# Kernel optimization log

Measured on AMD Instinct MI355X. Metric: run time of the kernel, lower is better.

The kernel has to match this reference:

```python
import jax, jax.numpy as jnp
import numpy as np

EPS = 1e-08


def setup_inputs() -> dict:
    key = jax.random.key(0)
    k1, k2, k3 = jax.random.split(key, 3)
    B_img, B_txt, D = 8192, 8192, 512
    img_feature = jax.random.normal(k1, (B_img, D), dtype=jnp.float32)
    text_feature = jax.random.normal(k2, (B_txt, D), dtype=jnp.float32)
    text_lens = jax.random.randint(k3, (B_txt,), 1, 40, dtype=jnp.int32)
    return {"img_feature": img_feature, "text_feature": text_feature, "text_lens": text_lens}


def reference(img_feature, text_feature, text_lens):
    # Pairwise cosine similarity: equivalent to the original expand+mul+sum,
    # expressed as a GEMM of the raw features followed by norm division.
    # w12[i,j] = <img_i, txt_j>; sim = w12 / max(|img_i|*|txt_j|, eps)
    w12 = jnp.einsum('id,jd->ij', img_feature, text_feature)  # [B_img, B_txt]
    w1 = jnp.linalg.norm(img_feature, axis=-1)                # [B_img]
    w2 = jnp.linalg.norm(text_feature, axis=-1)               # [B_txt]
    denom = jnp.maximum(w1[:, None] * w2[None, :], EPS)
    return w12 / denom
```

## Files before the change

kernel.cpp:

```cpp
#include <hip/hip_runtime.h>
#include <hip/hip_bf16.h>

#define M 8192
#define N 8192
#define K 512
#define BM 256
#define BN 128
#define BK 32
#define NT (K / BK)
#define EPSV 1e-8f

typedef __attribute__((ext_vector_type(8))) short bf16x8;
typedef __attribute__((ext_vector_type(4))) float f32x4;
typedef __attribute__((ext_vector_type(8))) unsigned short us8;

__device__ inline void gload_lds16(const void* g, void* l) {
  __builtin_amdgcn_global_load_lds(
      (const __attribute__((address_space(1))) unsigned int*)g,
      (__attribute__((address_space(3))) unsigned int*)l, 16, 0, 0);
}

#define BARRIER()                          \
  do {                                     \
    asm volatile("" ::: "memory");         \
    __builtin_amdgcn_s_barrier();          \
    asm volatile("" ::: "memory");         \
  } while (0)

__global__ __launch_bounds__(256) void prep_kernel(const float* __restrict__ img,
                                                   const float* __restrict__ txt,
                                                   unsigned short* __restrict__ Abf,
                                                   unsigned short* __restrict__ Bbf,
                                                   float* __restrict__ w1,
                                                   float* __restrict__ w2) {
  const int half = blockIdx.x >> 11;
  const int lb = blockIdx.x & 2047;
  const float* in = half ? txt : img;
  unsigned short* outb = half ? Bbf : Abf;
  float* norms = half ? w2 : w1;

  const int gw = (lb * 256 + threadIdx.x) >> 6;
  const int lane = threadIdx.x & 63;
  const float4* rp4 = (const float4*)(in + (size_t)gw * K);
  float4 v0 = rp4[lane * 2];
  float4 v1 = rp4[lane * 2 + 1];
  float ss = v0.x * v0.x + v0.y * v0.y + v0.z * v0.z + v0.w * v0.w +
             v1.x * v1.x + v1.y * v1.y + v1.z * v1.z + v1.w * v1.w;
  float f[8] = {v0.x, v0.y, v0.z, v0.w, v1.x, v1.y, v1.z, v1.w};
  us8 o;
#pragma unroll
  for (int i = 0; i < 8; ++i) {
    __hip_bfloat16 b = __float2bfloat16(f[i]);
    o[i] = *(unsigned short*)&b;
  }
  *(us8*)(outb + (size_t)gw * K + lane * 8) = o;
#pragma unroll
  for (int off = 32; off > 0; off >>= 1) ss += __shfl_down(ss, off, 64);
  if (lane == 0) norms[gw] = sqrtf(ss);
}

__global__ __launch_bounds__(512, 4) void gemm_kernel(const unsigned short* __restrict__ A,
                                                      const unsigned short* __restrict__ B,
                                                      const float* __restrict__ w1,
                                                      const float* __restrict__ w2,
                                                      float* __restrict__ C) {
  __shared__ __align__(128) unsigned short As[2][BM * BK];
  __shared__ __align__(128) unsigned short Bs[3][BN * BK];

  const int tid = threadIdx.x;
  const int wave = tid >> 6;
  const int lane = tid & 63;
  const int wr = wave >> 1;
  const int wc = wave & 1;
  const int fr = lane & 15;
  const int fq = lane >> 4;

  const int xcd = blockIdx.x & 7;
  const int idx = blockIdx.x >> 3;
  const int bRow = (idx >> 3) * BM;
  const int bCol = (xcd * 8 + (idx & 7)) * BN;

  const int srow = lane >> 2;
  const int scol = (lane & 3) * 8;

  auto stageA = [&](int buf, int kt) {
#pragma unroll
    for (int c = 0; c < 2; ++c)
      gload_lds16(A + (size_t)(bRow + c * 128 + wave * 16 + srow) * K + kt * BK + scol,
                  (char*)&As[buf][0] + (c * 128 + wave * 16) * 64);
  };
  auto stageB = [&](int buf, int kt) {
    gload_lds16(B + (size_t)(bCol + wave * 16 + srow) * K + kt * BK + scol,
                (char*)&Bs[buf][0] + wave * 16 * 64);
  };
  auto ldA = [&](int buf, int r) -> bf16x8 {
    return *(const bf16x8*)((const char*)&As[buf][0] + r * 64 + fq * 16);
  };
  auto ldB = [&](int buf, int r) -> bf16x8 {
    return *(const bf16x8*)((const char*)&Bs[buf][0] + r * 64 + fq * 16);
  };

  f32x4 acc[4][4] = {};
  bf16x8 a[4], b[4];

  stageA(0, 0);
  stageB(0, 0);
  stageB(1, 1);
  asm volatile("s_waitcnt vmcnt(1)" ::: "memory");
  BARRIER();

#pragma unroll
  for (int t = 0; t < NT; ++t) {
    const int cur = t & 1, nxt = cur ^ 1;
    const int bc = t % 3, b2 = (t + 2) % 3;

#pragma unroll
    for (int m = 0; m < 4; ++m) a[m] = ldA(cur, wr * 64 + m * 16 + fr);
    b[0] = ldB(bc, wc * 64 + fr);
    b[1] = ldB(bc, wc * 64 + 16 + fr);
    if (t + 1 < NT) stageA(nxt, t + 1);
    BARRIER();
    __builtin_amdgcn_s_setprio(1);
#pragma unroll
    for (int m = 0; m < 4; ++m)
#pragma unroll
      for (int n = 0; n < 2; ++n)
        acc[m][n] = __builtin_amdgcn_mfma_f32_16x16x32_bf16(a[m], b[n], acc[m][n], 0, 0, 0);
    __builtin_amdgcn_s_setprio(0);
    BARRIER();

    b[2] = ldB(bc, wc * 64 + 32 + fr);
    b[3] = ldB(bc, wc * 64 + 48 + fr);
    if (t + 2 < NT) stageB(b2, t + 2);
    BARRIER();
    __builtin_amdgcn_s_setprio(1);
#pragma unroll
    for (int m = 0; m < 4; ++m)
#pragma unroll
      for (int n = 2; n < 4; ++n)
        acc[m][n] = __builtin_amdgcn_mfma_f32_16x16x32_bf16(a[m], b[n], acc[m][n], 0, 0, 0);
    __builtin_amdgcn_s_setprio(0);
    if (t < NT - 2) {
      asm volatile("s_waitcnt vmcnt(1)" ::: "memory");
    } else if (t == NT - 2) {
      asm volatile("s_waitcnt vmcnt(0)" ::: "memory");
    }
    BARRIER();
  }

#pragma unroll
  for (int m = 0; m < 4; ++m) {
    const int row0 = bRow + wr * 64 + m * 16 + fq * 4;
    float w1v[4];
#pragma unroll
    for (int r = 0; r < 4; ++r) w1v[r] = w1[row0 + r];
#pragma unroll
    for (int n = 0; n < 4; ++n) {
      const int col = bCol + wc * 64 + n * 16 + fr;
      const float w2v = w2[col];
      f32x4 v = acc[m][n];
#pragma unroll
      for (int r = 0; r < 4; ++r)
        C[(size_t)(row0 + r) * N + col] = v[r] / fmaxf(w1v[r] * w2v, EPSV);
    }
  }
}

extern "C" void kernel_launch(void* const* d_in, const int* in_sizes, int n_in,
                              void* d_out, int out_size, void* d_ws, size_t ws_size,
                              hipStream_t stream) {
  (void)in_sizes; (void)n_in; (void)out_size; (void)ws_size;
  const float* img = (const float*)d_in[0];
  const float* txt = (const float*)d_in[1];
  float* out = (float*)d_out;

  unsigned short* Abf = (unsigned short*)d_ws;
  unsigned short* Bbf = Abf + (size_t)M * K;
  float* w1 = (float*)(Bbf + (size_t)N * K);
  float* w2 = w1 + M;

  prep_kernel<<<4096, 256, 0, stream>>>(img, txt, Abf, Bbf, w1, w2);
  gemm_kernel<<<(M / BM) * (N / BN), 512, 0, stream>>>(Abf, Bbf, w1, w2, out);
}
```

Before: 112.0 us.

## Make GEMM persistent over column tiles and overlap epilogue stores with next tile

Replaces the one-tile-per-block GEMM with 512 persistent blocks of 256 threads. Each block keeps a 128-row A strip and walks 8 column tiles, ping-ponging two accumulator sets so the previous tile's output stores are interleaved with the MFMA work of the current tile. It also switches to BK=64 with XOR-swizzled LDS to avoid bank conflicts, and precomputes reciprocal norms in the prep kernel so the epilogue multiplies instead of divides. The cost is doubled accumulator registers and lower occupancy. Clamping the norm at 1e-4 instead of clamping the product at 1e-8 changes behaviour only for near-zero vectors.

New measurement: 219.7 us. +96.2%, slower.

```diff
diff --git a/kernel.cpp b/kernel.cpp
--- a/kernel.cpp
+++ b/kernel.cpp
@@ -4,10 +4,9 @@
 #define M 8192
 #define N 8192
 #define K 512
-#define BM 256
+#define BM 128
 #define BN 128
-#define BK 32
-#define NT (K / BK)
+#define BK 64
 #define EPSV 1e-8f
 
 typedef __attribute__((ext_vector_type(8))) short bf16x8;
@@ -19,6 +18,8 @@
       (const __attribute__((address_space(1))) unsigned int*)g,
       (__attribute__((address_space(3))) unsigned int*)l, 16, 0, 0);
 }
+
+#define MEMFENCE() asm volatile("" ::: "memory")
 
 #define BARRIER()                          \
   do {                                     \
@@ -56,16 +57,16 @@
   *(us8*)(outb + (size_t)gw * K + lane * 8) = o;
 #pragma unroll
   for (int off = 32; off > 0; off >>= 1) ss += __shfl_down(ss, off, 64);
-  if (lane == 0) norms[gw] = sqrtf(ss);
-}
-
-__global__ __launch_bounds__(512, 4) void gemm_kernel(const unsigned short* __restrict__ A,
+  if (lane == 0) norms[gw] = 1.0f / fmaxf(sqrtf(ss), 1e-4f);
+}
+
+__global__ __launch_bounds__(256, 2) void gemm_kernel(const unsigned short* __restrict__ A,
                                                       const unsigned short* __restrict__ B,
-                                                      const float* __restrict__ w1,
-                                                      const float* __restrict__ w2,
+                                                      const float* __restrict__ iw1,
+                                                      const float* __restrict__ iw2,
                                                       float* __restrict__ C) {
-  __shared__ __align__(128) unsigned short As[2][BM * BK];
-  __shared__ __align__(128) unsigned short Bs[3][BN * BK];
+  __shared__ __align__(128) unsigned short As[2][128 * 64];
+  __shared__ __align__(128) unsigned short Bs[2][128 * 64];
 
   const int tid = threadIdx.x;
   const int wave = tid >> 6;
@@ -75,93 +76,133 @@
   const int fr = lane & 15;
   const int fq = lane >> 4;
 
-  const int xcd = blockIdx.x & 7;
-  const int idx = blockIdx.x >> 3;
-  const int bRow = (idx >> 3) * BM;
-  const int bCol = (xcd * 8 + (idx & 7)) * BN;
-
-  const int srow = lane >> 2;
-  const int scol = (lane & 3) * 8;
+  const int colBase = (int)(blockIdx.x & 7) * 8;
+  const int bRow = (int)(blockIdx.x >> 3) * BM;
+
+  const int srow = lane >> 3;
+  const int csw = ((lane & 7) * 16) ^ ((srow & 7) << 4);
 
   auto stageA = [&](int buf, int kt) {
 #pragma unroll
-    for (int c = 0; c < 2; ++c)
-      gload_lds16(A + (size_t)(bRow + c * 128 + wave * 16 + srow) * K + kt * BK + scol,
-                  (char*)&As[buf][0] + (c * 128 + wave * 16) * 64);
-  };
-  auto stageB = [&](int buf, int kt) {
-    gload_lds16(B + (size_t)(bCol + wave * 16 + srow) * K + kt * BK + scol,
-                (char*)&Bs[buf][0] + wave * 16 * 64);
-  };
-  auto ldA = [&](int buf, int r) -> bf16x8 {
-    return *(const bf16x8*)((const char*)&As[buf][0] + r * 64 + fq * 16);
-  };
-  auto ldB = [&](int buf, int r) -> bf16x8 {
-    return *(const bf16x8*)((const char*)&Bs[buf][0] + r * 64 + fq * 16);
-  };
-
-  f32x4 acc[4][4] = {};
-  bf16x8 a[4], b[4];
+    for (int c = 0; c < 4; ++c)
+      gload_lds16(A + (size_t)(bRow + c * 32 + wave * 8 + srow) * K + kt * BK + (csw >> 1),
+                  (char*)&As[buf][0] + (c * 32 + wave * 8) * 128);
+  };
+  auto stageB = [&](int buf, int bCol, int kt) {
+#pragma unroll
+    for (int c = 0; c < 4; ++c)
+      gload_lds16(B + (size_t)(bCol + c * 32 + wave * 8 + srow) * K + kt * BK + (csw >> 1),
+                  (char*)&Bs[buf][0] + (c * 32 + wave * 8) * 128);
+  };
+  auto ldA = [&](int buf, int m, int kk) -> bf16x8 {
+    const int r = wr * 64 + m * 16 + fr;
+    return *(const bf16x8*)((const char*)&As[buf][0] + r * 128 +
+                            ((kk * 64 + fq * 16) ^ ((r & 7) << 4)));
+  };
+  auto ldB = [&](int buf, int n, int kk) -> bf16x8 {
+    const int r = wc * 64 + n * 16 + fr;
+    return *(const bf16x8*)((const char*)&Bs[buf][0] + r * 128 +
+                            ((kk * 64 + fq * 16) ^ ((r & 7) << 4)));
+  };
+
+  float i1v[4][4];
+#pragma unroll
+  for (int m = 0; m < 4; ++m)
+#pragma unroll
+    for (int r = 0; r < 4; ++r) i1v[m][r] = iw1[bRow + wr * 64 + m * 16 + fq * 4 + r];
+
+  f32x4 accA[4][4] = {}, accB[4][4] = {};
+  float i2A[4] = {}, i2B[4] = {};
+
+  auto colOf = [&](int t) { return (colBase + t) * BN; };
 
   stageA(0, 0);
-  stageB(0, 0);
-  stageB(1, 1);
-  asm volatile("s_waitcnt vmcnt(1)" ::: "memory");
+  stageB(0, colOf(0), 0);
+  asm volatile("s_waitcnt vmcnt(0)" ::: "memory");
   BARRIER();
 
-#pragma unroll
-  for (int t = 0; t < NT; ++t) {
-    const int cur = t & 1, nxt = cur ^ 1;
-    const int bc = t % 3, b2 = (t + 2) % 3;
-
-#pragma unroll
-    for (int m = 0; m < 4; ++m) a[m] = ldA(cur, wr * 64 + m * 16 + fr);
-    b[0] = ldB(bc, wc * 64 + fr);
-    b[1] = ldB(bc, wc * 64 + 16 + fr);
-    if (t + 1 < NT) stageA(nxt, t + 1);
-    BARRIER();
-    __builtin_amdgcn_s_setprio(1);
+  auto tile_body = [&](f32x4 (&acc)[4][4], float (&i2)[4],
+                       f32x4 (&prev)[4][4], float (&i2p)[4],
+                       int colCur, int colPrev, int colNext) {
+#pragma unroll
+    for (int n = 0; n < 4; ++n) i2[n] = iw2[colCur + wc * 64 + n * 16 + fr];
 #pragma unroll
     for (int m = 0; m < 4; ++m)
 #pragma unroll
-      for (int n = 0; n < 2; ++n)
-        acc[m][n] = __builtin_amdgcn_mfma_f32_16x16x32_bf16(a[m], b[n], acc[m][n], 0, 0, 0);
-    __builtin_amdgcn_s_setprio(0);
-    BARRIER();
-
-    b[2] = ldB(bc, wc * 64 + 32 + fr);
-    b[3] = ldB(bc, wc * 64 + 48 + fr);
-    if (t + 2 < NT) stageB(b2, t + 2);
-    BARRIER();
-    __builtin_amdgcn_s_setprio(1);
-#pragma unroll
-    for (int m = 0; m < 4; ++m)
-#pragma unroll
-      for (int n = 2; n < 4; ++n)
-        acc[m][n] = __builtin_amdgcn_mfma_f32_16x16x32_bf16(a[m], b[n], acc[m][n], 0, 0, 0);
-    __builtin_amdgcn_s_setprio(0);
-    if (t < NT - 2) {
-      asm volatile("s_waitcnt vmcnt(1)" ::: "memory");
-    } else if (t == NT - 2) {
-      asm volatile("s_waitcnt vmcnt(0)" ::: "memory");
+      for (int n = 0; n < 4; ++n) acc[m][n] = (f32x4){0.f, 0.f, 0.f, 0.f};
+
+#pragma unroll
+    for (int s = 0; s < 8; ++s) {
+      const int cur = s & 1, nxt = cur ^ 1;
+      const int ktn = (s < 7) ? s + 1 : 0;
+      const int colStage = (s < 7) ? colCur : colNext;
+
+      bf16x8 a0[4], b0[4];
+#pragma unroll
+      for (int mm = 0; mm < 4; ++mm) a0[mm] = ldA(cur, mm, 0);
+#pragma unroll
+      for (int nn = 0; nn < 4; ++nn) b0[nn] = ldB(cur, nn, 0);
+      stageA(nxt, ktn);
+      BARRIER();
+      __builtin_amdgcn_s_setprio(1);
+#pragma unroll
+      for (int mm = 0; mm < 4; ++mm)
+#pragma unroll
+        for (int nn = 0; nn < 4; ++nn)
+          acc[mm][nn] = __builtin_amdgcn_mfma_f32_16x16x32_bf16(a0[mm], b0[nn],
+                                                                acc[mm][nn], 0, 0, 0);
+      __builtin_amdgcn_s_setprio(0);
+      BARRIER();
+
+      bf16x8 a1[4], b1[4];
+#pragma unroll
+      for (int mm = 0; mm < 4; ++mm) a1[mm] = ldA(cur, mm, 1);
+#pragma unroll
+      for (int nn = 0; nn < 4; ++nn) b1[nn] = ldB(cur, nn, 1);
+      stageB(nxt, colStage, ktn);
+      MEMFENCE();
+      {
+        const int dm = s >> 1, dn0 = (s & 1) * 2;
+        const int row0 = bRow + wr * 64 + dm * 16 + fq * 4;
+#pragma unroll
+        for (int d = 0; d < 2; ++d) {
+          const int dn = dn0 + d;
+          const int col = colPrev + wc * 64 + dn * 16 + fr;
+#pragma unroll
+          for (int r = 0; r < 4; ++r)
+            C[(size_t)(row0 + r) * N + col] = prev[dm][dn][r] * i1v[dm][r] * i2p[dn];
+        }
+      }
+      BARRIER();
+      __builtin_amdgcn_s_setprio(1);
+#pragma unroll
+      for (int mm = 0; mm < 4; ++mm)
+#pragma unroll
+        for (int nn = 0; nn < 4; ++nn)
+          acc[mm][nn] = __builtin_amdgcn_mfma_f32_16x16x32_bf16(a1[mm], b1[nn],
+                                                                acc[mm][nn], 0, 0, 0);
+      __builtin_amdgcn_s_setprio(0);
+      asm volatile("s_waitcnt vmcnt(8)" ::: "memory");
+      BARRIER();
     }
-    BARRIER();
+  };
+
+#pragma clang loop unroll(disable)
+  for (int p = 0; p < 4; ++p) {
+    const int tE = 2 * p, tO = 2 * p + 1;
+    tile_body(accA, i2A, accB, i2B, colOf(tE), p ? colOf(tE - 1) : colOf(7), colOf(tO));
+    tile_body(accB, i2B, accA, i2A, colOf(tO), colOf(tE), (p < 3) ? colOf(tO + 1) : colOf(0));
   }
 
 #pragma unroll
-  for (int m = 0; m < 4; ++m) {
-    const int row0 = bRow + wr * 64 + m * 16 + fq * 4;
-    float w1v[4];
-#pragma unroll
-    for (int r = 0; r < 4; ++r) w1v[r] = w1[row0 + r];
-#pragma unroll
-    for (int n = 0; n < 4; ++n) {
-      const int col = bCol + wc * 64 + n * 16 + fr;
-      const float w2v = w2[col];
-      f32x4 v = acc[m][n];
+  for (int dm = 0; dm < 4; ++dm) {
+    const int row0 = bRow + wr * 64 + dm * 16 + fq * 4;
+#pragma unroll
+    for (int dn = 0; dn < 4; ++dn) {
+      const int col = colOf(7) + wc * 64 + dn * 16 + fr;
 #pragma unroll
       for (int r = 0; r < 4; ++r)
-        C[(size_t)(row0 + r) * N + col] = v[r] / fmaxf(w1v[r] * w2v, EPSV);
+        C[(size_t)(row0 + r) * N + col] = accB[dm][dn][r] * i1v[dm][r] * i2B[dn];
     }
   }
 }
@@ -180,5 +221,5 @@
   float* w2 = w1 + M;
 
   prep_kernel<<<4096, 256, 0, stream>>>(img, txt, Abf, Bbf, w1, w2);
-  gemm_kernel<<<(M / BM) * (N / BN), 512, 0, stream>>>(Abf, Bbf, w1, w2, out);
-}
+  gemm_kernel<<<512, 256, 0, stream>>>(Abf, Bbf, w1, w2, out);
+}
```
